# Kernel tuning notes

Measured on AMD Instinct MI355X. Metric: run time of the kernel, lower is better.

## Reference

```python
import jax, jax.numpy as jnp
import numpy as np

T = 4096          # batch_size (time points)
C = 4096          # input_dims[1] == num_filters (channels/neurons)
FW = 64           # filter_width (temporal taps)


def setup_inputs() -> dict:
    key = jax.random.key(0)
    k1, k2, k3 = jax.random.split(key, 3)
    inputs = jax.random.normal(k1, (T, C), dtype=jnp.float32)
    weights = jax.random.uniform(k2, (FW, C), dtype=jnp.float32)
    biases = jax.random.normal(k3, (C,), dtype=jnp.float32) * 0.01
    return {"inputs": inputs, "weights": weights, "biases": biases}


def reference(inputs, weights, biases):
    # weight-norm (normalize_weights=1): per-filter L2 over taps, floored at 1e-8
    wnorms = jnp.maximum(jnp.sqrt(jnp.sum(jnp.square(weights), axis=0)), 1e-8)  # [C]
    filt = jnp.maximum(0.0, weights / wnorms)  # pos_constraint clamp, [FW, C]
    # Original does a full conv2d -> [C, T, 1, C] then takes the diagonal over
    # (batch-channel, filter-channel). Mathematically this is a per-channel
    # depthwise temporal SAME conv (cross-correlation, matching tf.nn.conv2d).
    x = inputs.T[None, :, :]            # [1, C, T]  (NCH)
    k = filt.T[:, None, :]              # [C, 1, FW] (OIH), group size 1
    pre = jax.lax.conv_general_dilated(
        x, k, window_strides=(1,), padding="SAME",
        feature_group_count=C,
        dimension_numbers=("NCH", "OIH", "NCH"))  # [1, C, T]
    # bias add; activation 'lin' = identity; ei_mask is None (num_inh=0)
    out = pre[0].T + biases[None, :]    # [T, C]
    return out
```

## Files before the change

### kernel.cpp

```cpp
#include <hip/hip_runtime.h>


#define T_DIM 4096
#define C_DIM 4096
#define FWID  64
#define PAD_L 31
#define KTILE 64
#define GRP   4

template <bool GUARD>
__device__ __forceinline__ void fir_body(const float* __restrict__ x,
                                         const float* __restrict__ w,
                                         const float* __restrict__ b,
                                         float* __restrict__ out,
                                         int c, int t0) {
    const float* __restrict__ xp = x + c;
    float* __restrict__ op = out + (long long)t0 * C_DIM + c;

    float wf[FWID];
    float ss = 0.0f;
#pragma unroll
    for (int f = 0; f < FWID; ++f) {
        wf[f] = w[f * C_DIM + c];
        ss = fmaf(wf[f], wf[f], ss);
    }
    const float inv = 1.0f / fmaxf(sqrtf(ss), 1e-8f);
#pragma unroll
    for (int f = 0; f < FWID; ++f) wf[f] = fmaxf(wf[f] * inv, 0.0f);

    const float bv = b[c];

    float xbuf[KTILE];
#pragma unroll
    for (int i = 0; i < KTILE; ++i) {
        const int m = t0 - PAD_L + i;
        const int s = (i + 33) & 63;
        if (!GUARD || ((unsigned)m < (unsigned)T_DIM))
            xbuf[s] = xp[(long long)m * C_DIM];
        else
            xbuf[s] = 0.0f;
    }

    float xnA[GRP], xnB[GRP];

#define PREFETCH(dst, g)                                                      \
    _Pragma("unroll")                                                         \
    for (int i = 0; i < GRP; ++i) {                                           \
        const int k = (g) * GRP + i;                                          \
        const int m = t0 + k + 33;                                            \
        float v = 0.0f;                                                       \
        if (k < KTILE - 1 && (!GUARD || m < T_DIM))                           \
            v = xp[(long long)m * C_DIM];                                     \
        dst[i] = v;                                                           \
    }

#define FIR_STEP(k, src)                                                      \
    {                                                                         \
        float a0 = bv, a1 = 0.0f, a2 = 0.0f, a3 = 0.0f;                       \
        _Pragma("unroll")                                                     \
        for (int f = 0; f < FWID; f += 4) {                                   \
            a0 = fmaf(wf[f + 0], xbuf[((k) + f + 33) & 63], a0);              \
            a1 = fmaf(wf[f + 1], xbuf[((k) + f + 34) & 63], a1);              \
            a2 = fmaf(wf[f + 2], xbuf[((k) + f + 35) & 63], a2);              \
            a3 = fmaf(wf[f + 3], xbuf[((k) + f + 36) & 63], a3);              \
        }                                                                     \
        __builtin_nontemporal_store((a0 + a1) + (a2 + a3),                    \
                                    op + (long long)(k) * C_DIM);             \
        if ((k) < KTILE - 1) xbuf[((k) + 33) & 63] = src[(k) & (GRP - 1)];    \
    }

#define GROUP(g, src)                                                         \
    FIR_STEP((g) * GRP + 0, src) FIR_STEP((g) * GRP + 1, src)                 \
    FIR_STEP((g) * GRP + 2, src) FIR_STEP((g) * GRP + 3, src)

    PREFETCH(xnA, 0)
    PREFETCH(xnB, 1)  GROUP(0,  xnA)
    PREFETCH(xnA, 2)  GROUP(1,  xnB)
    PREFETCH(xnB, 3)  GROUP(2,  xnA)
    PREFETCH(xnA, 4)  GROUP(3,  xnB)
    PREFETCH(xnB, 5)  GROUP(4,  xnA)
    PREFETCH(xnA, 6)  GROUP(5,  xnB)
    PREFETCH(xnB, 7)  GROUP(6,  xnA)
    PREFETCH(xnA, 8)  GROUP(7,  xnB)
    PREFETCH(xnB, 9)  GROUP(8,  xnA)
    PREFETCH(xnA, 10) GROUP(9,  xnB)
    PREFETCH(xnB, 11) GROUP(10, xnA)
    PREFETCH(xnA, 12) GROUP(11, xnB)
    PREFETCH(xnB, 13) GROUP(12, xnA)
    PREFETCH(xnA, 14) GROUP(13, xnB)
    PREFETCH(xnB, 15) GROUP(14, xnA)
    GROUP(15, xnB)

#undef GROUP
#undef FIR_STEP
#undef PREFETCH
}

__global__ __launch_bounds__(256, 3) void depthwise_fir_kernel(
    const float* __restrict__ x, const float* __restrict__ w,
    const float* __restrict__ b, float* __restrict__ out) {
    const int c  = blockIdx.y * 256 + threadIdx.x;
    const int t0 = blockIdx.x * KTILE;
    if (blockIdx.x == 0 || blockIdx.x == gridDim.x - 1)
        fir_body<true>(x, w, b, out, c, t0);
    else
        fir_body<false>(x, w, b, out, c, t0);
}

extern "C" void kernel_launch(void* const* d_in, const int* in_sizes, int n_in,
                              void* d_out, int out_size, void* d_ws, size_t ws_size,
                              hipStream_t stream) {
    const float* x = (const float*)d_in[0];
    const float* w = (const float*)d_in[1];
    const float* b = (const float*)d_in[2];
    float* out = (float*)d_out;

    dim3 grid(T_DIM / KTILE, C_DIM / 256);
    dim3 block(256);
    hipLaunchKernelGGL(depthwise_fir_kernel, grid, block, 0, stream, x, w, b, out);
}
```

Before: 51.84 us.

## Split filter taps across wave halves and combine partial sums via lane shuffle

Each channel is now handled by two lanes of a wave, each holding half of the 64 taps. Partial dot products are combined with a cross-half shuffle, and the two halves take turns storing alternate output rows. This halves per-thread register arrays to raise occupancy (launch bounds go from 3 to 4) and doubles the thread count. The cost is a shuffle per output, half of each 64-lane wave storing only 32 lanes at a time (narrower coalesced stores), and duplicated redundant x loads across the halves.

```diff
diff --git a/kernel.cpp b/kernel.cpp
--- a/kernel.cpp
+++ b/kernel.cpp
@@ -3,9 +3,9 @@
 
 #define T_DIM 4096
 #define C_DIM 4096
-#define FWID  64
 #define PAD_L 31
 #define KTILE 64
+#define HT    32
 #define GRP   4
 
 template <bool GUARD>
@@ -13,32 +13,35 @@
                                          const float* __restrict__ w,
                                          const float* __restrict__ b,
                                          float* __restrict__ out,
-                                         int c, int t0) {
+                                         int c, int half, int t0) {
     const float* __restrict__ xp = x + c;
+    const float* __restrict__ wp = w + half * HT * C_DIM + c;
     float* __restrict__ op = out + (long long)t0 * C_DIM + c;
 
-    float wf[FWID];
+    float wf[HT];
     float ss = 0.0f;
 #pragma unroll
-    for (int f = 0; f < FWID; ++f) {
-        wf[f] = w[f * C_DIM + c];
-        ss = fmaf(wf[f], wf[f], ss);
+    for (int j = 0; j < HT; ++j) {
+        wf[j] = wp[j * C_DIM];
+        ss = fmaf(wf[j], wf[j], ss);
     }
+    ss += __shfl_xor(ss, 32);
     const float inv = 1.0f / fmaxf(sqrtf(ss), 1e-8f);
 #pragma unroll
-    for (int f = 0; f < FWID; ++f) wf[f] = fmaxf(wf[f] * inv, 0.0f);
+    for (int j = 0; j < HT; ++j) wf[j] = fmaxf(wf[j] * inv, 0.0f);
 
-    const float bv = b[c];
+    const float bvseed = (half == 0) ? b[c] : 0.0f;
 
-    float xbuf[KTILE];
+    const int base = t0 - PAD_L + HT * half;
+
+    float xbuf[HT];
 #pragma unroll
-    for (int i = 0; i < KTILE; ++i) {
-        const int m = t0 - PAD_L + i;
-        const int s = (i + 33) & 63;
+    for (int i = 0; i < HT; ++i) {
+        const int m = base + i;
+        float v = 0.0f;
         if (!GUARD || ((unsigned)m < (unsigned)T_DIM))
-            xbuf[s] = xp[(long long)m * C_DIM];
-        else
-            xbuf[s] = 0.0f;
+            v = xp[(long long)m * C_DIM];
+        xbuf[(1 + i) & 31] = v;
     }
 
     float xnA[GRP], xnB[GRP];
@@ -47,26 +50,28 @@
     _Pragma("unroll")                                                         \
     for (int i = 0; i < GRP; ++i) {                                           \
         const int k = (g) * GRP + i;                                          \
-        const int m = t0 + k + 33;                                            \
+        const int m = base + k + HT;                                          \
         float v = 0.0f;                                                       \
-        if (k < KTILE - 1 && (!GUARD || m < T_DIM))                           \
+        if (k < KTILE - 1 && (!GUARD || ((unsigned)m < (unsigned)T_DIM)))     \
             v = xp[(long long)m * C_DIM];                                     \
         dst[i] = v;                                                           \
     }
 
 #define FIR_STEP(k, src)                                                      \
     {                                                                         \
-        float a0 = bv, a1 = 0.0f, a2 = 0.0f, a3 = 0.0f;                       \
+        float a0 = bvseed, a1 = 0.0f, a2 = 0.0f, a3 = 0.0f;                   \
         _Pragma("unroll")                                                     \
-        for (int f = 0; f < FWID; f += 4) {                                   \
-            a0 = fmaf(wf[f + 0], xbuf[((k) + f + 33) & 63], a0);              \
-            a1 = fmaf(wf[f + 1], xbuf[((k) + f + 34) & 63], a1);              \
-            a2 = fmaf(wf[f + 2], xbuf[((k) + f + 35) & 63], a2);              \
-            a3 = fmaf(wf[f + 3], xbuf[((k) + f + 36) & 63], a3);              \
+        for (int j = 0; j < HT; j += 4) {                                     \
+            a0 = fmaf(wf[j + 0], xbuf[((k) + j + 1) & 31], a0);               \
+            a1 = fmaf(wf[j + 1], xbuf[((k) + j + 2) & 31], a1);               \
+            a2 = fmaf(wf[j + 2], xbuf[((k) + j + 3) & 31], a2);               \
+            a3 = fmaf(wf[j + 3], xbuf[((k) + j + 4) & 31], a3);               \
         }                                                                     \
-        __builtin_nontemporal_store((a0 + a1) + (a2 + a3),                    \
-                                    op + (long long)(k) * C_DIM);             \
-        if ((k) < KTILE - 1) xbuf[((k) + 33) & 63] = src[(k) & (GRP - 1)];    \
+        float p = (a0 + a1) + (a2 + a3);                                      \
+        p += __shfl_xor(p, 32);                  \
+        if (half == ((k) & 1))                   \
+            __builtin_nontemporal_store(p, op + (long long)(k) * C_DIM);      \
+        if ((k) < KTILE - 1) xbuf[((k) + 1) & 31] = src[(k) & (GRP - 1)];     \
     }
 
 #define GROUP(g, src)                                                         \
@@ -96,15 +101,18 @@
 #undef PREFETCH
 }
 
-__global__ __launch_bounds__(256, 3) void depthwise_fir_kernel(
+__global__ __launch_bounds__(256, 4) void depthwise_fir_kernel(
     const float* __restrict__ x, const float* __restrict__ w,
     const float* __restrict__ b, float* __restrict__ out) {
-    const int c  = blockIdx.y * 256 + threadIdx.x;
-    const int t0 = blockIdx.x * KTILE;
+    const int lane = threadIdx.x & 63;
+    const int wave = threadIdx.x >> 6;
+    const int c    = blockIdx.y * 128 + wave * 32 + (lane & 31);
+    const int half = lane >> 5;
+    const int t0   = blockIdx.x * KTILE;
     if (blockIdx.x == 0 || blockIdx.x == gridDim.x - 1)
-        fir_body<true>(x, w, b, out, c, t0);
+        fir_body<true>(x, w, b, out, c, half, t0);
     else
-        fir_body<false>(x, w, b, out, c, t0);
+        fir_body<false>(x, w, b, out, c, half, t0);
 }
 
 extern "C" void kernel_launch(void* const* d_in, const int* in_sizes, int n_in,
@@ -115,7 +123,7 @@
     const float* b = (const float*)d_in[2];
     float* out = (float*)d_out;
 
-    dim3 grid(T_DIM / KTILE, C_DIM / 256);
+    dim3 grid(T_DIM / KTILE, C_DIM / 128);
     dim3 block(256);
     hipLaunchKernelGGL(depthwise_fir_kernel, grid, block, 0, stream, x, w, b, out);
 }
```

Measured after the change: 53.77 us. +3.7%, slower.
